# Kernel optimization log

Measured on AMD Instinct MI355X. Metric: run time of the kernel, lower is better.

Reference implementation:

```python
import jax, jax.numpy as jnp
import numpy as np

B, N, M = 32, 8400, 32
NUM_CLASSES = 80
TOP_K = 10
CLS_W, OBJ_W, REG_W = 1.0, 1.0, 5.0
EPS = 1e-7
IMG = 640.0


def setup_inputs() -> dict:
    key = jax.random.key(0)
    k1, k2, k3, k4, k5, k6, k7 = jax.random.split(key, 7)
    # decoded predictions in pixel scale: [cx, cy, w, h, obj_logit, cls_logits...]
    cxy = jax.random.uniform(k1, (B, N, 2), jnp.float32, 0.0, IMG)
    wh = jax.random.uniform(k2, (B, N, 2), jnp.float32, 10.0, 110.0)
    obj = jax.random.normal(k3, (B, N, 1), jnp.float32)
    cls = jax.random.normal(k4, (B, N, NUM_CLASSES), jnp.float32)
    predictions = jnp.concatenate([cxy, wh, obj, cls], axis=-1)  # (B, N, 85)
    # targets: [cls, cx, cy, w, h]
    gcls = jnp.floor(jax.random.uniform(k5, (B, M, 1), jnp.float32, 0.0, float(NUM_CLASSES)))
    gxy = jax.random.uniform(k6, (B, M, 2), jnp.float32, 50.0, IMG - 50.0)
    gwh = jax.random.uniform(k7, (B, M, 2), jnp.float32, 20.0, 120.0)
    targets = jnp.concatenate([gcls, gxy, gwh], axis=-1)  # (B, M, 5)
    return {"predictions": predictions, "targets": targets}


def cxcywh_to_xyxy(b):
    cx, cy, w, h = b[..., 0], b[..., 1], b[..., 2], b[..., 3]
    return jnp.stack([cx - w / 2, cy - h / 2, cx + w / 2, cy + h / 2], axis=-1)


def bce_with_logits(x, t):
    # numerically stable elementwise BCE with logits
    return jnp.maximum(x, 0.0) - x * t + jnp.log1p(jnp.exp(-jnp.abs(x)))


def pairwise_iou(g, p):
    # g: (M,4) xyxy, p: (N,4) xyxy -> (M,N)
    ix1 = jnp.maximum(g[:, None, 0], p[None, :, 0])
    iy1 = jnp.maximum(g[:, None, 1], p[None, :, 1])
    ix2 = jnp.minimum(g[:, None, 2], p[None, :, 2])
    iy2 = jnp.minimum(g[:, None, 3], p[None, :, 3])
    inter = jnp.clip(ix2 - ix1, 0.0) * jnp.clip(iy2 - iy1, 0.0)
    ga = jnp.clip(g[:, 2] - g[:, 0], 0.0) * jnp.clip(g[:, 3] - g[:, 1], 0.0)
    pa = jnp.clip(p[:, 2] - p[:, 0], 0.0) * jnp.clip(p[:, 3] - p[:, 1], 0.0)
    union = ga[:, None] + pa[None, :] - inter + EPS
    return inter / union


def giou(pred, tgt):
    # elementwise GIoU, pred/tgt (N,4) xyxy -> (N,)
    ix1 = jnp.maximum(pred[:, 0], tgt[:, 0]); iy1 = jnp.maximum(pred[:, 1], tgt[:, 1])
    ix2 = jnp.minimum(pred[:, 2], tgt[:, 2]); iy2 = jnp.minimum(pred[:, 3], tgt[:, 3])
    inter = jnp.clip(ix2 - ix1, 0.0) * jnp.clip(iy2 - iy1, 0.0)
    pa = jnp.clip(pred[:, 2] - pred[:, 0], 0.0) * jnp.clip(pred[:, 3] - pred[:, 1], 0.0)
    ta = jnp.clip(tgt[:, 2] - tgt[:, 0], 0.0) * jnp.clip(tgt[:, 3] - tgt[:, 1], 0.0)
    union = pa + ta - inter + EPS
    iou = inter / union
    ex1 = jnp.minimum(pred[:, 0], tgt[:, 0]); ey1 = jnp.minimum(pred[:, 1], tgt[:, 1])
    ex2 = jnp.maximum(pred[:, 2], tgt[:, 2]); ey2 = jnp.maximum(pred[:, 3], tgt[:, 3])
    enclose = (ex2 - ex1) * (ey2 - ey1) + EPS
    return iou - (enclose - union) / enclose


def _image_loss(pred, tgt):
    # pred: (N, 5+C), tgt: (M, 5)
    pbox = pred[:, :4]
    obj_logit = pred[:, 4]
    cls_logit = pred[:, 5:]
    pxyxy = cxcywh_to_xyxy(pbox)
    gcls = tgt[:, 0].astype(jnp.int32)                  # (M,)
    gxyxy = cxcywh_to_xyxy(tgt[:, 1:5])                 # (M,4)

    iou = pairwise_iou(gxyxy, pxyxy)                    # (M,N)

    # center prior: anchor (prediction) centers inside GT boxes
    cx, cy = pbox[:, 0], pbox[:, 1]
    in_box = ((cx[None, :] > gxyxy[:, 0:1]) & (cx[None, :] < gxyxy[:, 2:3]) &
              (cy[None, :] > gxyxy[:, 1:2]) & (cy[None, :] < gxyxy[:, 3:4]))  # (M,N)

    # classification cost: BCE(sqrt(cls_p*obj_p), onehot), decomposed to avoid (M,N,C)
    score = jnp.sqrt(jax.nn.sigmoid(cls_logit) * jax.nn.sigmoid(obj_logit)[:, None])  # (N,C)
    lp = jnp.log(score + EPS)
    lq = jnp.log(1.0 - score + EPS)
    base = -lq.sum(axis=-1)                             # (N,) = sum_c BCE(p, 0)
    cost_cls = base[None, :] - lp[:, gcls].T + lq[:, gcls].T  # (M,N)

    reg_cost = -jnp.log(iou + 1e-8)
    cost = cost_cls + 3.0 * reg_cost + 1e5 * (~in_box).astype(pred.dtype)
    cost = jax.lax.stop_gradient(cost)

    # dynamic-k: k_m = clip(sum of top-k IoUs, min 1)
    iou_sg = jax.lax.stop_gradient(iou) * in_box.astype(pred.dtype)
    topk_ious, _ = jax.lax.top_k(iou_sg, TOP_K)         # (M, TOP_K)
    dyn_k = jnp.clip(topk_ious.sum(-1).astype(jnp.int32), 1, None)  # (M,)

    # per-GT: keep the dyn_k lowest-cost candidates (rank via double argsort)
    ranks = jnp.argsort(jnp.argsort(cost, axis=1), axis=1)
    assigned = (ranks < dyn_k[:, None]) & in_box        # (M,N)

    # conflict resolution: anchor keeps only its lowest-cost GT
    big = jnp.asarray(1e30, pred.dtype)
    cost_masked = jnp.where(assigned, cost, big)
    matched_gt = jnp.argmin(cost_masked, axis=0)        # (N,)
    fg = assigned.any(axis=0)                            # (N,)
    fgf = fg.astype(pred.dtype)

    # objectness loss over all anchors
    obj_l = bce_with_logits(obj_logit, fgf).sum()
    # classification loss on foreground anchors
    onehot = jax.nn.one_hot(gcls[matched_gt], NUM_CLASSES, dtype=pred.dtype)
    cls_l = (bce_with_logits(cls_logit, onehot) * fgf[:, None]).sum()
    mbox = gxyxy[matched_gt]                            # (N,4)
    reg_l = ((1.0 - giou(pxyxy, mbox)) * fgf).sum()
    return cls_l, obj_l, reg_l, fgf.sum()


def reference(predictions, targets):
    cls_l, obj_l, reg_l, nfg = jax.vmap(_image_loss)(predictions, targets)
    num_fg = jnp.maximum(nfg.sum(), 1.0)
    total = (CLS_W * cls_l.sum() + OBJ_W * obj_l.sum() + REG_W * reg_l.sum()) / num_fg
    return total
```

## Files before the change

### kernel.cpp

```cpp
#include <hip/hip_runtime.h>
#include <math.h>

#define BB 32
#define NN 8400
#define MM 32
#define NC 80
#define PD 85
#define TOPK 10
#define CAP 2048
#define FLT_BIG 3.4e38f

__device__ __forceinline__ float bcef_(float x, float t) {
    return fmaxf(x, 0.0f) - x * t + log1pf(expf(-fabsf(x)));
}

__device__ __forceinline__ float frcp_(float x)  { return __builtin_amdgcn_rcpf(x); }
__device__ __forceinline__ float fsqrt_(float x) { return __builtin_amdgcn_sqrtf(x); }
__device__ __forceinline__ float fsig_(float x)  { return frcp_(1.0f + __expf(-x)); }

__device__ __forceinline__ float iou_(float4 pb, float gx1, float gy1,
                                      float gx2, float gy2, float ga) {
    float ix1 = fmaxf(gx1, pb.x), iy1 = fmaxf(gy1, pb.y);
    float ix2 = fminf(gx2, pb.z), iy2 = fminf(gy2, pb.w);
    float inter = fmaxf(ix2 - ix1, 0.0f) * fmaxf(iy2 - iy1, 0.0f);
    float pa = fmaxf(pb.z - pb.x, 0.0f) * fmaxf(pb.w - pb.y, 0.0f);
    float uni = ga + pa - inter + 1e-7f;
    return inter * frcp_(uni);
}
__device__ __forceinline__ float cost_(float cl, float so_n, float base_n, float iou) {
    float s = fsqrt_(fsig_(cl) * so_n);
    float lp = __logf(s + 1e-7f);
    float lq = __logf(1.0f - s + 1e-7f);
    return base_n - lp + lq - 3.0f * __logf(iou + 1e-8f);
}

__global__ void __launch_bounds__(256) kA(const float* __restrict__ pred,
                                          const float* __restrict__ tgt,
                                          float4* __restrict__ pxyxy,
                                          float* __restrict__ base,
                                          float* __restrict__ so,
                                          float* __restrict__ objlogit,
                                          unsigned int* __restrict__ inmask,
                                          unsigned int* __restrict__ mask) {
    const int tid = threadIdx.x;
    const int lane = tid & 63, wid = tid >> 6;
    const int rs = lane >> 5, g = lane & 31;
    const int b = blockIdx.y;
    const int tile = blockIdx.x;

    const float* t = tgt + ((size_t)b * MM + g) * 5;
    const float gx1 = t[1] - t[3] * 0.5f, gy1 = t[2] - t[4] * 0.5f;
    const float gx2 = t[1] + t[3] * 0.5f, gy2 = t[2] + t[4] * 0.5f;

    for (int itr = 0; itr < 2; ++itr) {
        const int pl = wid * 2 + itr;
        const int r0 = tile * 16 + pl * 2;
        const size_t off = ((size_t)b * NN + r0) * PD;

        float x0 = pred[off + lane];
        float x1 = pred[off + 64 + lane];

        float cx0 = __shfl(x0, 0), cy0 = __shfl(x0, 1), w0 = __shfl(x0, 2), h0 = __shfl(x0, 3), ol0 = __shfl(x0, 4);
        float cx1 = __shfl(x1, 21), cy1 = __shfl(x1, 22), w1 = __shfl(x1, 23), h1 = __shfl(x1, 24), ol1 = __shfl(x1, 25);
        float so0 = fsig_(ol0), so1 = fsig_(ol1);

        const float cxs = rs ? cx1 : cx0, cys = rs ? cy1 : cy0;
        const bool inb = (cxs > gx1) && (cxs < gx2) && (cys > gy1) && (cys < gy2);
        const unsigned long long bal = __ballot(inb);
        const bool r0a = (bal & 0xFFFFFFFFull) != 0ull;
        const bool r1a = (bal >> 32) != 0ull;

        const size_t gi = (size_t)b * NN + r0;
        if (lane == 0) {
            pxyxy[gi] = make_float4(cx0 - w0 * 0.5f, cy0 - h0 * 0.5f,
                                    cx0 + w0 * 0.5f, cy0 + h0 * 0.5f);
            objlogit[gi] = ol0; so[gi] = so0;
        } else if (lane == 1) {
            pxyxy[gi + 1] = make_float4(cx1 - w1 * 0.5f, cy1 - h1 * 0.5f,
                                        cx1 + w1 * 0.5f, cy1 + h1 * 0.5f);
            objlogit[gi + 1] = ol1; so[gi + 1] = so1;
        } else if (lane == 2) mask[gi] = 0u;
        else if (lane == 3) mask[gi + 1] = 0u;
        else if (lane == 4) inmask[gi] = (unsigned int)(bal & 0xFFFFFFFFull);
        else if (lane == 5) inmask[gi + 1] = (unsigned int)(bal >> 32);

        if (r0a) {
            float a0 = 0.0f;
            if (lane >= 5)  a0 += __logf(1.0f - fsqrt_(fsig_(x0) * so0) + 1e-7f);
            if (lane < 21)  a0 += __logf(1.0f - fsqrt_(fsig_(x1) * so0) + 1e-7f);
            #pragma unroll
            for (int o = 32; o; o >>= 1) a0 += __shfl_xor(a0, o);
            if (lane == 0) base[gi] = -a0;
        }
        if (r1a) {
            float x2 = (lane < 42) ? pred[off + 128 + lane] : 0.0f;
            float a1 = 0.0f;
            if (lane >= 26) a1 += __logf(1.0f - fsqrt_(fsig_(x1) * so1) + 1e-7f);
            if (lane < 42)  a1 += __logf(1.0f - fsqrt_(fsig_(x2) * so1) + 1e-7f);
            #pragma unroll
            for (int o = 32; o; o >>= 1) a1 += __shfl_xor(a1, o);
            if (lane == 0) base[gi + 1] = -a1;
        }
    }
}

__global__ void __launch_bounds__(256) kC(const float* __restrict__ pred,
                                          const float* __restrict__ tgt,
                                          const float4* __restrict__ pxyxy,
                                          const float* __restrict__ base,
                                          const float* __restrict__ so,
                                          const unsigned int* __restrict__ inmask,
                                          unsigned int* __restrict__ mask) {
    const int x_ = blockIdx.x & 7, k_ = blockIdx.x >> 3;
    const int g = k_ & 31, b = ((k_ >> 5) << 3) | x_;
    const int tid = threadIdx.x;
    const int wid = tid >> 6, lane = tid & 63;

    const float* t = tgt + ((size_t)b * MM + g) * 5;
    const int gcls = (int)t[0];
    const float gx1 = t[1] - t[3] * 0.5f, gy1 = t[2] - t[4] * 0.5f;
    const float gx2 = t[1] + t[3] * 0.5f, gy2 = t[2] + t[4] * 0.5f;
    const float ga = fmaxf(gx2 - gx1, 0.0f) * fmaxf(gy2 - gy1, 0.0f);
    const size_t nb = (size_t)b * NN;
    const unsigned int gbit = 1u << g;

    __shared__ float s_iou[CAP];
    __shared__ float s_cost[CAP];
    __shared__ int   s_n[CAP];
    __shared__ int   s_cnt;
    if (tid == 0) s_cnt = 0;
    __syncthreads();

    for (int n = tid; n < NN; n += 256) {
        if (inmask[nb + n] & gbit) {
            float4 pb = pxyxy[nb + n];
            float iou = iou_(pb, gx1, gy1, gx2, gy2, ga);
            float cl = pred[(nb + (size_t)n) * PD + 5 + gcls];
            float co = cost_(cl, so[nb + n], base[nb + n], iou);
            int idx = atomicAdd(&s_cnt, 1);
            if (idx < CAP) { s_iou[idx] = iou; s_cost[idx] = co; s_n[idx] = n; }
        }
    }
    __syncthreads();

    if (wid != 0) return;
    const int cnt = min(s_cnt, CAP);

    float ssum = 0.0f;
    {
        unsigned int consumed = 0u;
        const int lim = (cnt < TOPK) ? cnt : TOPK;
        for (int p = 0; p < lim; ++p) {
            float bv = -1.0f; int bidx = 0x7fffffff;
            int k = 0;
            for (int i = lane; i < cnt; i += 64, ++k) {
                if (!((consumed >> k) & 1u)) {
                    float v = s_iou[i];
                    if (v > bv) { bv = v; bidx = i; }
                }
            }
            #pragma unroll
            for (int o = 32; o; o >>= 1) {
                float ov = __shfl_xor(bv, o); int oi = __shfl_xor(bidx, o);
                if (ov > bv || (ov == bv && oi < bidx)) { bv = ov; bidx = oi; }
            }
            ssum += bv;
            if ((bidx & 63) == lane) consumed |= 1u << (bidx >> 6);
        }
    }
    int dynk = (int)ssum;
    if (dynk < 1) dynk = 1;
    if (dynk > TOPK) dynk = TOPK;

    {
        unsigned int consumed = 0u;
        const int lim = (cnt < dynk) ? cnt : dynk;
        for (int p = 0; p < lim; ++p) {
            float bv = FLT_BIG; int bn_ = 0x7fffffff; int bidx = -1;
            int k = 0;
            for (int i = lane; i < cnt; i += 64, ++k) {
                if (!((consumed >> k) & 1u)) {
                    float v = s_cost[i]; int n_ = s_n[i];
                    if (v < bv || (v == bv && n_ < bn_)) { bv = v; bn_ = n_; bidx = i; }
                }
            }
            #pragma unroll
            for (int o = 32; o; o >>= 1) {
                float ov = __shfl_xor(bv, o);
                int on = __shfl_xor(bn_, o);
                int oi = __shfl_xor(bidx, o);
                if (ov < bv || (ov == bv && on < bn_)) { bv = ov; bn_ = on; bidx = oi; }
            }
            if ((bidx & 63) == lane) consumed |= 1u << (bidx >> 6);
            if (lane == 0) atomicOr(&mask[nb + bn_], gbit);
        }
    }
}

__global__ void __launch_bounds__(256) kD(const float* __restrict__ pred,
                   const float* __restrict__ tgt,
                   const float4* __restrict__ pxyxy,
                   const float* __restrict__ base,
                   const float* __restrict__ so,
                   const float* __restrict__ objlogit,
                   const unsigned int* __restrict__ mask,
                   float* __restrict__ partials) {
    const int tid = threadIdx.x;
    const int i0 = blockIdx.x * 256;
    const int i = i0 + tid;
    const int lane = tid & 63, wid = tid >> 6;
    const int b = i / NN;

    float obj_l, cls_l = 0.0f, reg_l = 0.0f, nfg = 0.0f;
    const unsigned int mk = mask[i];
    obj_l = bcef_(objlogit[i], mk ? 1.0f : 0.0f);

    __shared__ int s_list[256];
    __shared__ int s_gcls[256];
    __shared__ int s_wbase[4];
    __shared__ int s_cnt;

    unsigned long long bal = __ballot(mk != 0);
    int wpos = __popcll(bal & ((1ull << lane) - 1ull));
    if (lane == 0) s_wbase[wid] = __popcll(bal);
    __syncthreads();
    if (tid == 0) {
        int acc = 0;
        for (int w = 0; w < 4; ++w) { int t_ = s_wbase[w]; s_wbase[w] = acc; acc += t_; }
        s_cnt = acc;
    }
    __syncthreads();

    if (mk) {
        int e = s_wbase[wid] + wpos;
        s_list[e] = tid;
        nfg = 1.0f;
        float4 pb = pxyxy[i];
        float base_n = base[i], so_n = so[i];
        float best = 3.0e30f; int bg = 0;
        for (int g = 0; g < MM; ++g) {
            if ((mk >> g) & 1u) {
                const float* tg = tgt + ((size_t)b * MM + g) * 5;
                float ggx1 = tg[1] - tg[3] * 0.5f, ggy1 = tg[2] - tg[4] * 0.5f;
                float ggx2 = tg[1] + tg[3] * 0.5f, ggy2 = tg[2] + tg[4] * 0.5f;
                float gga = fmaxf(ggx2 - ggx1, 0.0f) * fmaxf(ggy2 - ggy1, 0.0f);
                float iou = iou_(pb, ggx1, ggy1, ggx2, ggy2, gga);
                float cl = pred[(size_t)i * PD + 5 + (int)tg[0]];
                float cvv = cost_(cl, so_n, base_n, iou);
                if (cvv < best) { best = cvv; bg = g; }
            }
        }
        const float* tm = tgt + ((size_t)b * MM + bg) * 5;
        s_gcls[e] = (int)tm[0];
        float px1 = pb.x, py1 = pb.y, px2 = pb.z, py2 = pb.w;
        float tx1 = tm[1] - tm[3] * 0.5f, ty1 = tm[2] - tm[4] * 0.5f;
        float tx2 = tm[1] + tm[3] * 0.5f, ty2 = tm[2] + tm[4] * 0.5f;
        float ix1 = fmaxf(px1, tx1), iy1 = fmaxf(py1, ty1);
        float ix2 = fminf(px2, tx2), iy2 = fminf(py2, ty2);
        float inter = fmaxf(ix2 - ix1, 0.0f) * fmaxf(iy2 - iy1, 0.0f);
        float pa = fmaxf(px2 - px1, 0.0f) * fmaxf(py2 - py1, 0.0f);
        float ta = fmaxf(tx2 - tx1, 0.0f) * fmaxf(ty2 - ty1, 0.0f);
        float uni = pa + ta - inter + 1e-7f;
        float iou = inter / uni;
        float ex1 = fminf(px1, tx1), ey1 = fminf(py1, ty1);
        float ex2 = fmaxf(px2, tx2), ey2 = fmaxf(py2, ty2);
        float enclose = (ex2 - ex1) * (ey2 - ey1) + 1e-7f;
        float giou = iou - (enclose - uni) / enclose;
        reg_l = 1.0f - giou;
    }
    __syncthreads();

    const int cnt = s_cnt;
    const int nitems = cnt * NC;
    for (int item = tid; item < nitems; item += 256) {
        int e = item / NC;
        int c = item - e * NC;
        int gi = i0 + s_list[e];
        float x = pred[(size_t)gi * PD + 5 + c];
        cls_l += bcef_(x, (c == s_gcls[e]) ? 1.0f : 0.0f);
    }

    __shared__ float red[256];
    float sums[4] = {cls_l, obj_l, reg_l, nfg};
    float out4[4];
    for (int j = 0; j < 4; ++j) {
        red[tid] = sums[j];
        __syncthreads();
        for (int off = 128; off > 0; off >>= 1) {
            if (tid < off) red[tid] += red[tid + off];
            __syncthreads();
        }
        out4[j] = red[0];
        __syncthreads();
    }
    if (tid == 0) {
        float* pr = partials + (size_t)blockIdx.x * 4;
        pr[0] = out4[0]; pr[1] = out4[1]; pr[2] = out4[2]; pr[3] = out4[3];
    }
}

__global__ void kE(const float* __restrict__ partials, int nblk, float* __restrict__ out) {
    __shared__ float red[256];
    float s[4] = {0, 0, 0, 0};
    for (int i = threadIdx.x; i < nblk; i += 256) {
        s[0] += partials[(size_t)i * 4 + 0];
        s[1] += partials[(size_t)i * 4 + 1];
        s[2] += partials[(size_t)i * 4 + 2];
        s[3] += partials[(size_t)i * 4 + 3];
    }
    float tot[4];
    for (int j = 0; j < 4; ++j) {
        red[threadIdx.x] = s[j];
        __syncthreads();
        for (int off = 128; off > 0; off >>= 1) {
            if (threadIdx.x < off) red[threadIdx.x] += red[threadIdx.x + off];
            __syncthreads();
        }
        tot[j] = red[0];
        __syncthreads();
    }
    if (threadIdx.x == 0) {
        float nfg = fmaxf(tot[3], 1.0f);
        out[0] = (tot[0] + tot[1] + 5.0f * tot[2]) / nfg;
    }
}

extern "C" void kernel_launch(void* const* d_in, const int* in_sizes, int n_in,
                              void* d_out, int out_size, void* d_ws, size_t ws_size,
                              hipStream_t stream) {
    const float* pred = (const float*)d_in[0];
    const float* tgt  = (const float*)d_in[1];
    float* out = (float*)d_out;

    char* ws = (char*)d_ws;
    size_t off = 0;
    float4* pxyxy = (float4*)(ws + off);            off += (size_t)BB * NN * sizeof(float4);
    float* base = (float*)(ws + off);               off += (size_t)BB * NN * sizeof(float);
    float* so = (float*)(ws + off);                 off += (size_t)BB * NN * sizeof(float);
    float* objlogit = (float*)(ws + off);           off += (size_t)BB * NN * sizeof(float);
    unsigned int* inmask = (unsigned int*)(ws + off); off += (size_t)BB * NN * sizeof(unsigned int);
    unsigned int* mask = (unsigned int*)(ws + off); off += (size_t)BB * NN * sizeof(unsigned int);
    float* partials = (float*)(ws + off);

    const int nblk = (BB * NN + 255) / 256;

    dim3 gA(NN / 16, BB);
    kA<<<gA, 256, 0, stream>>>(pred, tgt, pxyxy, base, so, objlogit, inmask, mask);

    kC<<<MM * BB, 256, 0, stream>>>(pred, tgt, pxyxy, base, so, inmask, mask);

    kD<<<nblk, 256, 0, stream>>>(pred, tgt, pxyxy, base, so, objlogit, mask, partials);

    kE<<<1, 256, 0, stream>>>(partials, nblk, out);
}
```

Measured before the change: 95.44 us.

## Build per-GT candidate lists in kA via global atomics, shrink kC to compaction readers

```diff
diff --git a/kernel.cpp b/kernel.cpp
--- a/kernel.cpp
+++ b/kernel.cpp
@@ -7,7 +7,7 @@
 #define NC 80
 #define PD 85
 #define TOPK 10
-#define CAP 2048
+#define CAPG 768
 #define FLT_BIG 3.4e38f
 
 __device__ __forceinline__ float bcef_(float x, float t) {
@@ -40,8 +40,10 @@
                                           float* __restrict__ base,
                                           float* __restrict__ so,
                                           float* __restrict__ objlogit,
-                                          unsigned int* __restrict__ inmask,
-                                          unsigned int* __restrict__ mask) {
+                                          unsigned int* __restrict__ mask,
+                                          float2* __restrict__ candA,
+                                          int* __restrict__ candN,
+                                          int* __restrict__ cntg) {
     const int tid = threadIdx.x;
     const int lane = tid & 63, wid = tid >> 6;
     const int rs = lane >> 5, g = lane & 31;
@@ -49,8 +51,12 @@
     const int tile = blockIdx.x;
 
     const float* t = tgt + ((size_t)b * MM + g) * 5;
+    const int gcls = (int)t[0];
     const float gx1 = t[1] - t[3] * 0.5f, gy1 = t[2] - t[4] * 0.5f;
     const float gx2 = t[1] + t[3] * 0.5f, gy2 = t[2] + t[4] * 0.5f;
+    const float ga = fmaxf(gx2 - gx1, 0.0f) * fmaxf(gy2 - gy1, 0.0f);
+    const int posn = rs * 85 + 5 + gcls;
+    const int pk = posn >> 6, ls = posn & 63;
 
     for (int itr = 0; itr < 2; ++itr) {
         const int pl = wid * 2 + itr;
@@ -59,6 +65,7 @@
 
         float x0 = pred[off + lane];
         float x1 = pred[off + 64 + lane];
+        float x2 = 0.0f;
 
         float cx0 = __shfl(x0, 0), cy0 = __shfl(x0, 1), w0 = __shfl(x0, 2), h0 = __shfl(x0, 3), ol0 = __shfl(x0, 4);
         float cx1 = __shfl(x1, 21), cy1 = __shfl(x1, 22), w1 = __shfl(x1, 23), h1 = __shfl(x1, 24), ol1 = __shfl(x1, 25);
@@ -81,70 +88,69 @@
             objlogit[gi + 1] = ol1; so[gi + 1] = so1;
         } else if (lane == 2) mask[gi] = 0u;
         else if (lane == 3) mask[gi + 1] = 0u;
-        else if (lane == 4) inmask[gi] = (unsigned int)(bal & 0xFFFFFFFFull);
-        else if (lane == 5) inmask[gi + 1] = (unsigned int)(bal >> 32);
-
+
+        float base0 = 0.0f, base1 = 0.0f;
         if (r0a) {
             float a0 = 0.0f;
             if (lane >= 5)  a0 += __logf(1.0f - fsqrt_(fsig_(x0) * so0) + 1e-7f);
             if (lane < 21)  a0 += __logf(1.0f - fsqrt_(fsig_(x1) * so0) + 1e-7f);
             #pragma unroll
             for (int o = 32; o; o >>= 1) a0 += __shfl_xor(a0, o);
-            if (lane == 0) base[gi] = -a0;
+            base0 = -a0;
+            if (lane == 0) base[gi] = base0;
         }
         if (r1a) {
-            float x2 = (lane < 42) ? pred[off + 128 + lane] : 0.0f;
+            x2 = (lane < 42) ? pred[off + 128 + lane] : 0.0f;
             float a1 = 0.0f;
             if (lane >= 26) a1 += __logf(1.0f - fsqrt_(fsig_(x1) * so1) + 1e-7f);
             if (lane < 42)  a1 += __logf(1.0f - fsqrt_(fsig_(x2) * so1) + 1e-7f);
             #pragma unroll
             for (int o = 32; o; o >>= 1) a1 += __shfl_xor(a1, o);
-            if (lane == 0) base[gi + 1] = -a1;
-        }
-    }
-}
-
-__global__ void __launch_bounds__(256) kC(const float* __restrict__ pred,
-                                          const float* __restrict__ tgt,
-                                          const float4* __restrict__ pxyxy,
-                                          const float* __restrict__ base,
-                                          const float* __restrict__ so,
-                                          const unsigned int* __restrict__ inmask,
-                                          unsigned int* __restrict__ mask) {
-    const int x_ = blockIdx.x & 7, k_ = blockIdx.x >> 3;
-    const int g = k_ & 31, b = ((k_ >> 5) << 3) | x_;
-    const int tid = threadIdx.x;
-    const int wid = tid >> 6, lane = tid & 63;
-
-    const float* t = tgt + ((size_t)b * MM + g) * 5;
-    const int gcls = (int)t[0];
-    const float gx1 = t[1] - t[3] * 0.5f, gy1 = t[2] - t[4] * 0.5f;
-    const float gx2 = t[1] + t[3] * 0.5f, gy2 = t[2] + t[4] * 0.5f;
-    const float ga = fmaxf(gx2 - gx1, 0.0f) * fmaxf(gy2 - gy1, 0.0f);
+            base1 = -a1;
+            if (lane == 0) base[gi + 1] = base1;
+        }
+
+        if (bal != 0ull) {
+            float g0 = __shfl(x0, ls), g1 = __shfl(x1, ls), g2 = __shfl(x2, ls);
+            float cl = (pk == 0) ? g0 : ((pk == 1) ? g1 : g2);
+            if (inb) {
+                const float ws_ = rs ? w1 : w0, hs_ = rs ? h1 : h0;
+                const float sos = rs ? so1 : so0, bases = rs ? base1 : base0;
+                float4 pb = make_float4(cxs - ws_ * 0.5f, cys - hs_ * 0.5f,
+                                        cxs + ws_ * 0.5f, cys + hs_ * 0.5f);
+                float iou = iou_(pb, gx1, gy1, gx2, gy2, ga);
+                float co = cost_(cl, sos, bases, iou);
+                int bg = (b << 5) + g;
+                int idx = atomicAdd(&cntg[bg], 1);
+                if (idx < CAPG) {
+                    candA[(size_t)bg * CAPG + idx] = make_float2(co, iou);
+                    candN[(size_t)bg * CAPG + idx] = r0 + rs;
+                }
+            }
+        }
+    }
+}
+
+__global__ void __launch_bounds__(64) kC(const float2* __restrict__ candA,
+                                         const int* __restrict__ candN,
+                                         const int* __restrict__ cntg,
+                                         unsigned int* __restrict__ mask) {
+    const int bg = blockIdx.x;
+    const int b = bg >> 5, g = bg & 31;
+    const int lane = threadIdx.x;
     const size_t nb = (size_t)b * NN;
     const unsigned int gbit = 1u << g;
 
-    __shared__ float s_iou[CAP];
-    __shared__ float s_cost[CAP];
-    __shared__ int   s_n[CAP];
-    __shared__ int   s_cnt;
-    if (tid == 0) s_cnt = 0;
+    const int cnt = min(cntg[bg], CAPG);
+    __shared__ float s_iou[CAPG];
+    __shared__ float s_cost[CAPG];
+    __shared__ int   s_n[CAPG];
+    for (int i = lane; i < cnt; i += 64) {
+        float2 e = candA[(size_t)bg * CAPG + i];
+        s_cost[i] = e.x; s_iou[i] = e.y;
+        s_n[i] = candN[(size_t)bg * CAPG + i];
+    }
     __syncthreads();
-
-    for (int n = tid; n < NN; n += 256) {
-        if (inmask[nb + n] & gbit) {
-            float4 pb = pxyxy[nb + n];
-            float iou = iou_(pb, gx1, gy1, gx2, gy2, ga);
-            float cl = pred[(nb + (size_t)n) * PD + 5 + gcls];
-            float co = cost_(cl, so[nb + n], base[nb + n], iou);
-            int idx = atomicAdd(&s_cnt, 1);
-            if (idx < CAP) { s_iou[idx] = iou; s_cost[idx] = co; s_n[idx] = n; }
-        }
-    }
-    __syncthreads();
-
-    if (wid != 0) return;
-    const int cnt = min(s_cnt, CAP);
 
     float ssum = 0.0f;
     {
@@ -338,16 +344,21 @@
     float* base = (float*)(ws + off);               off += (size_t)BB * NN * sizeof(float);
     float* so = (float*)(ws + off);                 off += (size_t)BB * NN * sizeof(float);
     float* objlogit = (float*)(ws + off);           off += (size_t)BB * NN * sizeof(float);
-    unsigned int* inmask = (unsigned int*)(ws + off); off += (size_t)BB * NN * sizeof(unsigned int);
     unsigned int* mask = (unsigned int*)(ws + off); off += (size_t)BB * NN * sizeof(unsigned int);
+    float2* candA = (float2*)(ws + off);            off += (size_t)BB * MM * CAPG * sizeof(float2);
+    int* candN = (int*)(ws + off);                  off += (size_t)BB * MM * CAPG * sizeof(int);
+    int* cntg = (int*)(ws + off);                   off += (size_t)BB * MM * sizeof(int);
     float* partials = (float*)(ws + off);
 
     const int nblk = (BB * NN + 255) / 256;
 
+    hipMemsetAsync(cntg, 0, (size_t)BB * MM * sizeof(int), stream);
+
     dim3 gA(NN / 16, BB);
-    kA<<<gA, 256, 0, stream>>>(pred, tgt, pxyxy, base, so, objlogit, inmask, mask);
-
-    kC<<<MM * BB, 256, 0, stream>>>(pred, tgt, pxyxy, base, so, inmask, mask);
+    kA<<<gA, 256, 0, stream>>>(pred, tgt, pxyxy, base, so, objlogit, mask,
+                               candA, candN, cntg);
+
+    kC<<<MM * BB, 64, 0, stream>>>(candA, candN, cntg, mask);
 
     kD<<<nblk, 256, 0, stream>>>(pred, tgt, pxyxy, base, so, objlogit, mask, partials);
 
```

New measurement: 177.1 us. 85.6% more time.
